# Performance work log

Measured on AMD Instinct MI355X. Metric: run time of the kernel, lower is better.

Reference implementation:

```python
import jax, jax.numpy as jnp
import numpy as np

B, N, E, H, P = 4, 512, 512, 32, 128
D = E // H
SCALING = D ** -0.5
EPS = 1e-5


def layer_norm(x, g, b):
    mu = jnp.mean(x, axis=-1, keepdims=True)
    var = jnp.var(x, axis=-1, keepdims=True)
    return (x - mu) * jax.lax.rsqrt(var + EPS) * g + b


def setup_inputs() -> dict:
    key = jax.random.key(0)
    ks = jax.random.split(key, 12)
    inp = {
        "query": jax.random.normal(ks[0], (B, N, E), jnp.float32),
        "pair": jax.random.normal(ks[1], (B, N, N, P), jnp.float32),
        "attn_mask": jnp.zeros((B, H, N, N), jnp.float32),
        "delta_pos": jax.random.normal(ks[2], (B, N, N, 3), jnp.float32),
        # parameters
        "ln_g": jnp.ones((E,), jnp.float32),
        "ln_b": jnp.zeros((E,), jnp.float32),
        "Wq": jax.random.normal(ks[3], (E, E), jnp.float32) * (1.0 / np.sqrt(E)),
        "Wk": jax.random.normal(ks[4], (E, E), jnp.float32) * (1.0 / np.sqrt(E)),
        "Wv": jax.random.normal(ks[5], (E, E), jnp.float32) * (1.0 / np.sqrt(E)),
        "pln_g": jnp.ones((P,), jnp.float32),
        "pln_b": jnp.zeros((P,), jnp.float32),
        "Wb": jax.random.normal(ks[6], (H, P), jnp.float32) * (1.0 / np.sqrt(P)),
        "bb": jnp.zeros((H,), jnp.float32),
        "Wf": jax.random.normal(ks[7], (1, E), jnp.float32) * (1.0 / np.sqrt(E)),
    }
    return inp


def reference(query, pair, attn_mask, delta_pos,
              ln_g, ln_b, Wq, Wk, Wv, pln_g, pln_b, Wb, bb, Wf):
    x = layer_norm(query, ln_g, ln_b)                       # (B,N,E)
    q = (x @ Wq.T).reshape(B, N, H, D).transpose(0, 2, 1, 3) * SCALING  # (B,H,N,D)
    k = (x @ Wk.T).reshape(B, N, H, D).transpose(0, 2, 1, 3)
    v = (x @ Wv.T).reshape(B, N, H, D).transpose(0, 2, 1, 3)
    attn = jnp.einsum('bhid,bhjd->bhij', q, k)              # (B,H,N,N)
    pair_n = layer_norm(pair, pln_g, pln_b)
    bias = (pair_n @ Wb.T + bb).transpose(0, 3, 1, 2)       # (B,H,N,N)
    attn = jax.nn.softmax(attn + bias + attn_mask, axis=-1)  # dropout off (eval)
    # rot_attn_probs: attn (B,H,N,N) * delta_pos (B,N,N,3) -> contract over j with v
    # out per (b, i, coord c, head h, d): sum_j attn[b,h,i,j]*delta_pos[b,i,j,c]*v[b,h,j,d]
    xo = jnp.einsum('bhij,bijc,bhjd->bichd', attn, delta_pos, v)  # (B,N,3,H,D)
    xo = xo.reshape(B, N, 3, E)
    cur_force = (xo @ Wf.T).reshape(B, N, 3)
    return cur_force
```

## Files before the change

kernel.cpp:

```cpp
#include <hip/hip_runtime.h>
#include <hip/hip_bf16.h>
#include <stdint.h>

constexpr int cB = 4, cN = 512, cE = 512, cH = 32, cP = 128;

typedef __attribute__((ext_vector_type(8))) short bf16x8;
typedef __attribute__((ext_vector_type(4))) float f32x4;

__device__ __forceinline__ unsigned short f2bf(float f) {
    union { float f; unsigned u; } v; v.f = f;
    unsigned u = v.u;
    u += 0x7fffu + ((u >> 16) & 1u);
    return (unsigned short)(u >> 16);
}
__device__ __forceinline__ float bf2f(unsigned short s) {
    union { unsigned u; float f; } v; v.u = ((unsigned)s) << 16;
    return v.f;
}

__global__ __launch_bounds__(256) void ln_query_kernel(
    const float* __restrict__ q, const float* __restrict__ g,
    const float* __restrict__ b, float* __restrict__ xn)
{
    int row = blockIdx.x;
    int t = threadIdx.x;
    const float* xr = q + (size_t)row * cE;
    float2 v = *(const float2*)(xr + t * 2);
    float s = v.x + v.y;
    float ss = v.x * v.x + v.y * v.y;
    #pragma unroll
    for (int o = 32; o > 0; o >>= 1) {
        s  += __shfl_down(s, o, 64);
        ss += __shfl_down(ss, o, 64);
    }
    __shared__ float red[8];
    int wv = t >> 6, ln = t & 63;
    if (ln == 0) { red[wv] = s; red[wv + 4] = ss; }
    __syncthreads();
    if (t == 0) {
        float S = red[0] + red[1] + red[2] + red[3];
        float SS = red[4] + red[5] + red[6] + red[7];
        float mu = S * (1.0f / cE);
        float var = SS * (1.0f / cE) - mu * mu;
        red[0] = mu; red[1] = rsqrtf(var + 1e-5f);
    }
    __syncthreads();
    float mu = red[0], rs = red[1];
    float2 gg = *(const float2*)(g + t * 2);
    float2 bb2 = *(const float2*)(b + t * 2);
    float2 o2;
    o2.x = (v.x - mu) * rs * gg.x + bb2.x;
    o2.y = (v.y - mu) * rs * gg.y + bb2.y;
    *(float2*)(xn + (size_t)row * cE + t * 2) = o2;
}

__global__ void setup_kernel(
    const float* __restrict__ Wb, const float* __restrict__ pg,
    const float* __restrict__ pb, const float* __restrict__ bbv,
    unsigned short* __restrict__ Wbp, float* __restrict__ Sh,
    float* __restrict__ cbh)
{
    int h = threadIdx.x;
    if (h < cH) {
        float s = 0.f, c = bbv[h];
        for (int p = 0; p < cP; ++p) {
            float wv = Wb[h * cP + p];
            float wp = wv * pg[p];
            s += wp;
            c += pb[p] * wv;
            Wbp[h * cP + p] = f2bf(wp);
        }
        Sh[h] = s; cbh[h] = c;
    }
}

__global__ __launch_bounds__(256) void qkv_kernel(
    const float* __restrict__ xn,
    const float* __restrict__ Wq, const float* __restrict__ Wk,
    const float* __restrict__ Wv, const float* __restrict__ Wf,
    float* __restrict__ Q, float* __restrict__ K, float* __restrict__ w)
{
    int mtile = blockIdx.x & 31;
    int ntile = blockIdx.x >> 5;
    int mat = ntile >> 3;
    int ncol0 = (ntile & 7) * 64;
    const float* W = (mat == 0) ? Wq : ((mat == 1) ? Wk : Wv);
    int rm = mtile * 64;
    int t = threadIdx.x;
    int tm = t >> 4, tn = t & 15;

    __shared__ float As[32][68];
    __shared__ float Bs[32][68];
    float acc[4][4];
    #pragma unroll
    for (int i = 0; i < 4; ++i)
        #pragma unroll
        for (int j = 0; j < 4; ++j) acc[i][j] = 0.f;

    for (int k0 = 0; k0 < cE; k0 += 32) {
        #pragma unroll
        for (int s = 0; s < 2; ++s) {
            int f = t + 256 * s;
            int row = f >> 3, kq = f & 7;
            float4 v = *(const float4*)(xn + (size_t)(rm + row) * cE + k0 + kq * 4);
            As[kq * 4 + 0][row] = v.x; As[kq * 4 + 1][row] = v.y;
            As[kq * 4 + 2][row] = v.z; As[kq * 4 + 3][row] = v.w;
            float4 u = *(const float4*)(W + (size_t)(ncol0 + row) * cE + k0 + kq * 4);
            Bs[kq * 4 + 0][row] = u.x; Bs[kq * 4 + 1][row] = u.y;
            Bs[kq * 4 + 2][row] = u.z; Bs[kq * 4 + 3][row] = u.w;
        }
        __syncthreads();
        #pragma unroll
        for (int kk = 0; kk < 32; ++kk) {
            float a[4], bv[4];
            #pragma unroll
            for (int i = 0; i < 4; ++i) a[i] = As[kk][tm * 4 + i];
            #pragma unroll
            for (int j = 0; j < 4; ++j) bv[j] = Bs[kk][tn * 4 + j];
            #pragma unroll
            for (int i = 0; i < 4; ++i)
                #pragma unroll
                for (int j = 0; j < 4; ++j) acc[i][j] = fmaf(a[i], bv[j], acc[i][j]);
        }
        __syncthreads();
    }

    if (mat < 2) {
        float scale = (mat == 0) ? 0.25f : 1.0f;
        float* dst = (mat == 0) ? Q : K;
        #pragma unroll
        for (int i = 0; i < 4; ++i) {
            int r = rm + tm * 4 + i;
            float4 o;
            o.x = acc[i][0] * scale; o.y = acc[i][1] * scale;
            o.z = acc[i][2] * scale; o.w = acc[i][3] * scale;
            *(float4*)(dst + (size_t)r * cE + ncol0 + tn * 4) = o;
        }
    } else {
        int col0 = ncol0 + tn * 4;
        int h = col0 >> 4;
        float wf[4];
        #pragma unroll
        for (int j = 0; j < 4; ++j) wf[j] = Wf[col0 + j];
        #pragma unroll
        for (int i = 0; i < 4; ++i) {
            int r = rm + tm * 4 + i;
            float part = 0.f;
            #pragma unroll
            for (int j = 0; j < 4; ++j) part = fmaf(acc[i][j], wf[j], part);
            atomicAdd(&w[(size_t)r * cH + h], part);
        }
    }
}

__global__ __launch_bounds__(256, 4) void attn_kernel(
    const float* __restrict__ pair, const float* __restrict__ mask,
    const float* __restrict__ dpos, const float* __restrict__ Q,
    const float* __restrict__ K, const float* __restrict__ w,
    const unsigned short* __restrict__ Wbp, const float* __restrict__ Sh_g,
    const float* __restrict__ cb_g, float* __restrict__ out)
{
    int bi = blockIdx.x;
    int b = bi >> 9, i = bi & 511;
    int t = threadIdx.x;
    int lane = t & 63, wv = t >> 6;

    __shared__ __align__(16) unsigned short Ap[64 * 136];
    __shared__ __align__(16) unsigned short Bw[32 * 136];
    __shared__ float biasT[64 * 33];
    __shared__ float mrow[64], rrow[64];
    __shared__ __align__(16) float dl2[2][192];
    __shared__ float statred[64][8];

    {
        const ushort4* src = (const ushort4*)Wbp;
        #pragma unroll
        for (int s = 0; s < 4; ++s) {
            int f = t + 256 * s;
            int hh = f >> 5, p4 = f & 31;
            ushort4 v = src[f];
            *(ushort4*)&Bw[hh * 136 + p4 * 4] = v;
        }
    }

    int h = t & 31, js = t >> 5;
    int g = js, c4 = t & 31;

    float qreg[16];
    {
        const float4* qp = (const float4*)(Q + (size_t)bi * cE + h * 16);
        #pragma unroll
        for (int d4 = 0; d4 < 4; ++d4) {
            float4 qv = qp[d4];
            qreg[d4 * 4 + 0] = qv.x; qreg[d4 * 4 + 1] = qv.y;
            qreg[d4 * 4 + 2] = qv.z; qreg[d4 * 4 + 3] = qv.w;
        }
    }
    float Sh_loc = Sh_g[h], cb_loc = cb_g[h];

    float m = -1e30f, l = 0.f, a0 = 0.f, a1 = 0.f, a2 = 0.f;

    const float* pbase = pair + (size_t)bi * cN * cP;
    const float* dbase = dpos + (size_t)bi * cN * 3;
    const float* Kbase = K + (size_t)b * cN * cE;
    const float* wbase = w + (size_t)b * cN * cH;
    const float* mbase = mask + ((size_t)(b * cH + h) * cN + i) * cN;

    float4 pf[8];
    #pragma unroll
    for (int s = 0; s < 8; ++s)
        pf[s] = *(const float4*)(pbase + (size_t)(g + 8 * s) * cP + c4 * 4);
    float4 dpf = {0.f, 0.f, 0.f, 0.f};
    if (t < 48) dpf = *(const float4*)(dbase + t * 4);

    for (int it = 0; it < 8; ++it) {
        int j0 = it * 64;
        int buf = it & 1;

        #pragma unroll
        for (int s = 0; s < 8; ++s) {
            ushort4 u;
            u.x = f2bf(pf[s].x); u.y = f2bf(pf[s].y);
            u.z = f2bf(pf[s].z); u.w = f2bf(pf[s].w);
            *(ushort4*)&Ap[(g + 8 * s) * 136 + c4 * 4] = u;
        }
        if (t < 48) *(float4*)&dl2[buf][t * 4] = dpf;

        if (it < 7) {
            const float* pb2 = pbase + (size_t)(j0 + 64) * cP;
            #pragma unroll
            for (int s = 0; s < 8; ++s)
                pf[s] = *(const float4*)(pb2 + (size_t)(g + 8 * s) * cP + c4 * 4);
            if (t < 48) dpf = *(const float4*)(dbase + (size_t)(j0 + 64) * 3 + t * 4);
        }

        float mka[8];
        {
            float4 mf0 = *(const float4*)(mbase + j0 + js * 8);
            float4 mf1 = *(const float4*)(mbase + j0 + js * 8 + 4);
            mka[0] = mf0.x; mka[1] = mf0.y; mka[2] = mf0.z; mka[3] = mf0.w;
            mka[4] = mf1.x; mka[5] = mf1.y; mka[6] = mf1.z; mka[7] = mf1.w;
        }

        __syncthreads();

        {
            int r = t >> 2, q = t & 3;
            float s1 = 0.f, s2 = 0.f;
            #pragma unroll
            for (int p = 0; p < 32; ++p) {
                float f = bf2f(Ap[r * 136 + q * 32 + p]);
                s1 += f; s2 = fmaf(f, f, s2);
            }
            statred[r][q] = s1; statred[r][q + 4] = s2;
        }

        {
            f32x4 acc0 = {0.f, 0.f, 0.f, 0.f}, acc1 = {0.f, 0.f, 0.f, 0.f};
            int arow = wv * 16 + (lane & 15);
            int kq = (lane >> 4) * 8;
            #pragma unroll
            for (int kb = 0; kb < 4; ++kb) {
                int k = kb * 32 + kq;
                bf16x8 af = *(const bf16x8*)&Ap[arow * 136 + k];
                bf16x8 b0 = *(const bf16x8*)&Bw[(lane & 15) * 136 + k];
                bf16x8 b1 = *(const bf16x8*)&Bw[(16 + (lane & 15)) * 136 + k];
                acc0 = __builtin_amdgcn_mfma_f32_16x16x32_bf16(af, b0, acc0, 0, 0, 0);
                acc1 = __builtin_amdgcn_mfma_f32_16x16x32_bf16(af, b1, acc1, 0, 0, 0);
            }
            int crow = wv * 16 + (lane >> 4) * 4;
            int ccol = lane & 15;
            #pragma unroll
            for (int r = 0; r < 4; ++r) {
                biasT[(crow + r) * 33 + ccol] = acc0[r];
                biasT[(crow + r) * 33 + 16 + ccol] = acc1[r];
            }
        }
        __syncthreads();

        if (t < 64) {
            float s1 = statred[t][0] + statred[t][1] + statred[t][2] + statred[t][3];
            float s2 = statred[t][4] + statred[t][5] + statred[t][6] + statred[t][7];
            float mu = s1 * (1.0f / cP);
            float var = s2 * (1.0f / cP) - mu * mu;
            mrow[t] = mu;
            rrow[t] = rsqrtf(var + 1e-5f);
        }
        __syncthreads();

        #pragma unroll
        for (int jj = 0; jj < 8; ++jj) {
            int jr = js * 8 + jj;
            int j = j0 + jr;
            float bias = rrow[jr] * (biasT[jr * 33 + h] - mrow[jr] * Sh_loc) + cb_loc;
            const float4* kp4 = (const float4*)(Kbase + (size_t)j * cE + h * 16);
            float qk = 0.f;
            #pragma unroll
            for (int d4 = 0; d4 < 4; ++d4) {
                float4 kv = kp4[d4];
                qk = fmaf(qreg[d4 * 4 + 0], kv.x, qk);
                qk = fmaf(qreg[d4 * 4 + 1], kv.y, qk);
                qk = fmaf(qreg[d4 * 4 + 2], kv.z, qk);
                qk = fmaf(qreg[d4 * 4 + 3], kv.w, qk);
            }
            float z = qk + bias + mka[jj];
            float wj = wbase[(size_t)j * cH + h];
            float mn = fmaxf(m, z);
            float sc = __expf(m - mn);
            float p = __expf(z - mn);
            l = l * sc + p;
            float pw = p * wj;
            a0 = fmaf(pw, dl2[buf][jr * 3 + 0], a0 * sc);
            a1 = fmaf(pw, dl2[buf][jr * 3 + 1], a1 * sc);
            a2 = fmaf(pw, dl2[buf][jr * 3 + 2], a2 * sc);
            m = mn;
        }
    }

    __syncthreads();
    float* red = biasT;
    red[(h * 8 + js) * 6 + 0] = m;
    red[(h * 8 + js) * 6 + 1] = l;
    red[(h * 8 + js) * 6 + 2] = a0;
    red[(h * 8 + js) * 6 + 3] = a1;
    red[(h * 8 + js) * 6 + 4] = a2;
    __syncthreads();
    for (int s = 4; s >= 1; s >>= 1) {
        if (js < s) {
            float* p1 = &red[(h * 8 + js) * 6];
            float* p2 = &red[(h * 8 + js + s) * 6];
            float m1 = p1[0], m2 = p2[0];
            float mn = fmaxf(m1, m2);
            float s1 = __expf(m1 - mn), s2 = __expf(m2 - mn);
            p1[0] = mn;
            p1[1] = p1[1] * s1 + p2[1] * s2;
            p1[2] = p1[2] * s1 + p2[2] * s2;
            p1[3] = p1[3] * s1 + p2[3] * s2;
            p1[4] = p1[4] * s1 + p2[4] * s2;
        }
        __syncthreads();
    }
    if (js == 0) {
        float linv = 1.0f / red[h * 48 + 1];
        biasT[1536 + h * 3 + 0] = red[h * 48 + 2] * linv;
        biasT[1536 + h * 3 + 1] = red[h * 48 + 3] * linv;
        biasT[1536 + h * 3 + 2] = red[h * 48 + 4] * linv;
    }
    __syncthreads();
    if (t < 3) {
        float s = 0.f;
        #pragma unroll
        for (int hh = 0; hh < cH; ++hh) s += biasT[1536 + hh * 3 + t];
        out[(size_t)bi * 3 + t] = s;
    }
}

extern "C" void kernel_launch(void* const* d_in, const int* in_sizes, int n_in,
                              void* d_out, int out_size, void* d_ws, size_t ws_size,
                              hipStream_t stream)
{
    const float* query = (const float*)d_in[0];
    const float* pair  = (const float*)d_in[1];
    const float* amask = (const float*)d_in[2];
    const float* dpos  = (const float*)d_in[3];
    const float* ln_g  = (const float*)d_in[4];
    const float* ln_b  = (const float*)d_in[5];
    const float* Wq    = (const float*)d_in[6];
    const float* Wk    = (const float*)d_in[7];
    const float* Wv    = (const float*)d_in[8];
    const float* pg    = (const float*)d_in[9];
    const float* pb    = (const float*)d_in[10];
    const float* Wb    = (const float*)d_in[11];
    const float* bbv   = (const float*)d_in[12];
    const float* Wf    = (const float*)d_in[13];
    float* out = (float*)d_out;

    char* ws = (char*)d_ws;
    float* xn = (float*)ws;
    float* Q  = (float*)(ws + (size_t)4 * 1048576);
    float* K  = (float*)(ws + (size_t)8 * 1048576);
    float* w  = (float*)(ws + (size_t)12 * 1048576);
    unsigned short* Wbp = (unsigned short*)(ws + (size_t)12 * 1048576 + 262144);
    float* Sh  = (float*)(ws + (size_t)12 * 1048576 + 262144 + 8192);
    float* cbh = (float*)(ws + (size_t)12 * 1048576 + 262144 + 8192 + 128);

    ln_query_kernel<<<cB * cN, 256, 0, stream>>>(query, ln_g, ln_b, xn);
    setup_kernel<<<1, 64, 0, stream>>>(Wb, pg, pb, bbv, Wbp, Sh, cbh);
    hipMemsetAsync(w, 0, (size_t)cB * cN * cH * sizeof(float), stream);
    qkv_kernel<<<32 * 24, 256, 0, stream>>>(xn, Wq, Wk, Wv, Wf, Q, K, w);
    attn_kernel<<<cB * cN, 256, 0, stream>>>(pair, amask, dpos, Q, K, w, Wbp, Sh, cbh, out);
}
```

Measured before the change: 1.012 ms.

## Replace syncthreads with non-draining barriers and prefetch mask and weights

Adds a barrier that waits only on LDS counters, so outstanding global prefetches of pair/dpos/mask stay in flight across the barrier instead of being drained by __syncthreads. The mask row is now prefetched one iteration ahead, and the per-j w values are loaded into registers early. The layernorm statistics reduction uses wave shuffles in place of a shared-memory array, which removes one barrier per iteration. The LDS stat reads are vectorized. Register pressure rises, and correctness depends on the compiler inserting vmcnt waits before the prefetched values are used.

```diff
diff --git a/kernel.cpp b/kernel.cpp
--- a/kernel.cpp
+++ b/kernel.cpp
@@ -16,6 +16,13 @@
 __device__ __forceinline__ float bf2f(unsigned short s) {
     union { unsigned u; float f; } v; v.u = ((unsigned)s) << 16;
     return v.f;
+}
+
+__device__ __forceinline__ void barrier_nodrain() {
+    asm volatile("s_waitcnt lgkmcnt(0)" ::: "memory");
+    __builtin_amdgcn_sched_barrier(0);
+    __builtin_amdgcn_s_barrier();
+    __builtin_amdgcn_sched_barrier(0);
 }
 
 __global__ __launch_bounds__(256) void ln_query_kernel(
@@ -170,7 +177,6 @@
     __shared__ float biasT[64 * 33];
     __shared__ float mrow[64], rrow[64];
     __shared__ __align__(16) float dl2[2][192];
-    __shared__ float statred[64][8];
 
     {
         const ushort4* src = (const ushort4*)Wbp;
@@ -206,6 +212,8 @@
     const float* wbase = w + (size_t)b * cN * cH;
     const float* mbase = mask + ((size_t)(b * cH + h) * cN + i) * cN;
 
+    float4 mk0 = *(const float4*)(mbase + js * 8);
+    float4 mk1 = *(const float4*)(mbase + js * 8 + 4);
     float4 pf[8];
     #pragma unroll
     for (int s = 0; s < 8; ++s)
@@ -226,7 +234,20 @@
         }
         if (t < 48) *(float4*)&dl2[buf][t * 4] = dpf;
 
+        float mka[8];
+        mka[0] = mk0.x; mka[1] = mk0.y; mka[2] = mk0.z; mka[3] = mk0.w;
+        mka[4] = mk1.x; mka[5] = mk1.y; mka[6] = mk1.z; mka[7] = mk1.w;
+
+        float wreg[8];
+        #pragma unroll
+        for (int jj = 0; jj < 8; ++jj)
+            wreg[jj] = wbase[(size_t)(j0 + js * 8 + jj) * cH + h];
+
+        __builtin_amdgcn_sched_barrier(0);
+
         if (it < 7) {
+            mk0 = *(const float4*)(mbase + j0 + 64 + js * 8);
+            mk1 = *(const float4*)(mbase + j0 + 64 + js * 8 + 4);
             const float* pb2 = pbase + (size_t)(j0 + 64) * cP;
             #pragma unroll
             for (int s = 0; s < 8; ++s)
@@ -234,27 +255,35 @@
             if (t < 48) dpf = *(const float4*)(dbase + (size_t)(j0 + 64) * 3 + t * 4);
         }
 
-        float mka[8];
-        {
-            float4 mf0 = *(const float4*)(mbase + j0 + js * 8);
-            float4 mf1 = *(const float4*)(mbase + j0 + js * 8 + 4);
-            mka[0] = mf0.x; mka[1] = mf0.y; mka[2] = mf0.z; mka[3] = mf0.w;
-            mka[4] = mf1.x; mka[5] = mf1.y; mka[6] = mf1.z; mka[7] = mf1.w;
-        }
-
-        __syncthreads();
+        barrier_nodrain();
 
         {
             int r = t >> 2, q = t & 3;
+            const uint4* apv = (const uint4*)&Ap[r * 136 + q * 32];
             float s1 = 0.f, s2 = 0.f;
             #pragma unroll
-            for (int p = 0; p < 32; ++p) {
-                float f = bf2f(Ap[r * 136 + q * 32 + p]);
-                s1 += f; s2 = fmaf(f, f, s2);
+            for (int vv = 0; vv < 4; ++vv) {
+                uint4 x = apv[vv];
+                unsigned uu[4] = {x.x, x.y, x.z, x.w};
+                #pragma unroll
+                for (int e = 0; e < 4; ++e) {
+                    union { unsigned u; float f; } lo, hi;
+                    lo.u = uu[e] << 16;
+                    hi.u = uu[e] & 0xffff0000u;
+                    s1 += lo.f + hi.f;
+                    s2 = fmaf(lo.f, lo.f, s2);
+                    s2 = fmaf(hi.f, hi.f, s2);
+                }
             }
-            statred[r][q] = s1; statred[r][q + 4] = s2;
-        }
-
+            s1 += __shfl_xor(s1, 1, 64); s2 += __shfl_xor(s2, 1, 64);
+            s1 += __shfl_xor(s1, 2, 64); s2 += __shfl_xor(s2, 2, 64);
+            if ((t & 3) == 0) {
+                float mu = s1 * (1.0f / cP);
+                float var = s2 * (1.0f / cP) - mu * mu;
+                mrow[r] = mu;
+                rrow[r] = rsqrtf(var + 1e-5f);
+            }
+        }
         {
             f32x4 acc0 = {0.f, 0.f, 0.f, 0.f}, acc1 = {0.f, 0.f, 0.f, 0.f};
             int arow = wv * 16 + (lane & 15);
@@ -276,17 +305,8 @@
                 biasT[(crow + r) * 33 + 16 + ccol] = acc1[r];
             }
         }
-        __syncthreads();
-
-        if (t < 64) {
-            float s1 = statred[t][0] + statred[t][1] + statred[t][2] + statred[t][3];
-            float s2 = statred[t][4] + statred[t][5] + statred[t][6] + statred[t][7];
-            float mu = s1 * (1.0f / cP);
-            float var = s2 * (1.0f / cP) - mu * mu;
-            mrow[t] = mu;
-            rrow[t] = rsqrtf(var + 1e-5f);
-        }
-        __syncthreads();
+
+        barrier_nodrain();
 
         #pragma unroll
         for (int jj = 0; jj < 8; ++jj) {
@@ -304,7 +324,7 @@
                 qk = fmaf(qreg[d4 * 4 + 3], kv.w, qk);
             }
             float z = qk + bias + mka[jj];
-            float wj = wbase[(size_t)j * cH + h];
+            float wj = wreg[jj];
             float mn = fmaxf(m, z);
             float sc = __expf(m - mn);
             float p = __expf(z - mn);
```

Result: slower. 1.064 ms (+5.2%).

## Stream pair tiles via global_load_lds and normalize in-tile before MFMA bias

Applied to the files above, without the earlier changes.

The attention kernel now loads 32-row pair tiles straight into LDS with global_load_lds, in place of staging them in registers. It layer-normalizes each row in fp32 before converting to bf16, so the MFMA output is the bias directly and the separate stats/mean-correction passes and extra barriers go away. Work is remapped so each thread owns one head and 4 j values from the MFMA accumulator, with mask and w values prefetched one tile ahead. Custom barriers with explicit waitcnt replace __syncthreads. The trade is more iterations (16 vs 8) and a single-buffered LDS tile that is overwritten while computing, which relies on the barrier ordering being correct.

```diff
diff --git a/kernel.cpp b/kernel.cpp
--- a/kernel.cpp
+++ b/kernel.cpp
@@ -13,9 +13,26 @@
     u += 0x7fffu + ((u >> 16) & 1u);
     return (unsigned short)(u >> 16);
 }
-__device__ __forceinline__ float bf2f(unsigned short s) {
-    union { unsigned u; float f; } v; v.u = ((unsigned)s) << 16;
-    return v.f;
+__device__ __forceinline__ unsigned pack2bf(float lo, float hi) {
+    return (unsigned)f2bf(lo) | ((unsigned)f2bf(hi) << 16);
+}
+
+#define BAR_VM() do { \
+    asm volatile("s_waitcnt vmcnt(0) lgkmcnt(0)" ::: "memory"); \
+    __builtin_amdgcn_sched_barrier(0); \
+    __builtin_amdgcn_s_barrier(); \
+    __builtin_amdgcn_sched_barrier(0); } while (0)
+
+#define BAR_LGKM() do { \
+    asm volatile("s_waitcnt lgkmcnt(0)" ::: "memory"); \
+    __builtin_amdgcn_sched_barrier(0); \
+    __builtin_amdgcn_s_barrier(); \
+    __builtin_amdgcn_sched_barrier(0); } while (0)
+
+__device__ __forceinline__ void gl_lds16(const float* g, float* l) {
+    __builtin_amdgcn_global_load_lds(
+        (const __attribute__((address_space(1))) void*)g,
+        (__attribute__((address_space(3))) void*)l, 16, 0, 0);
 }
 
 __global__ __launch_bounds__(256) void ln_query_kernel(
@@ -54,24 +71,31 @@
     *(float2*)(xn + (size_t)row * cE + t * 2) = o2;
 }
 
-__global__ void setup_kernel(
+__global__ __launch_bounds__(256) void setup_kernel(
     const float* __restrict__ Wb, const float* __restrict__ pg,
     const float* __restrict__ pb, const float* __restrict__ bbv,
     unsigned short* __restrict__ Wbp, float* __restrict__ Sh,
     float* __restrict__ cbh)
 {
-    int h = threadIdx.x;
-    if (h < cH) {
-        float s = 0.f, c = bbv[h];
-        for (int p = 0; p < cP; ++p) {
-            float wv = Wb[h * cP + p];
-            float wp = wv * pg[p];
-            s += wp;
-            c += pb[p] * wv;
-            Wbp[h * cP + p] = f2bf(wp);
-        }
-        Sh[h] = s; cbh[h] = c;
-    }
+    int t = threadIdx.x;
+    int h = t >> 3, s8 = t & 7;
+    const float* wrow = Wb + h * cP + s8 * 16;
+    const float* pgp = pg + s8 * 16;
+    const float* pbp = pb + s8 * 16;
+    unsigned short* wdst = Wbp + h * cP + s8 * 16;
+    float s = 0.f, c = 0.f;
+    #pragma unroll
+    for (int e = 0; e < 16; ++e) {
+        float wv = wrow[e];
+        float wp = wv * pgp[e];
+        s += wp;
+        c = fmaf(pbp[e], wv, c);
+        wdst[e] = f2bf(wp);
+    }
+    s += __shfl_xor(s, 1, 64); c += __shfl_xor(c, 1, 64);
+    s += __shfl_xor(s, 2, 64); c += __shfl_xor(c, 2, 64);
+    s += __shfl_xor(s, 4, 64); c += __shfl_xor(c, 4, 64);
+    if (s8 == 0) { Sh[h] = s; cbh[h] = c + bbv[h]; }
 }
 
 __global__ __launch_bounds__(256) void qkv_kernel(
@@ -165,12 +189,10 @@
     int t = threadIdx.x;
     int lane = t & 63, wv = t >> 6;
 
-    __shared__ __align__(16) unsigned short Ap[64 * 136];
+    __shared__ __align__(16) float Lf32[4096];
+    __shared__ __align__(16) unsigned short Ap[32 * 136];
     __shared__ __align__(16) unsigned short Bw[32 * 136];
-    __shared__ float biasT[64 * 33];
-    __shared__ float mrow[64], rrow[64];
-    __shared__ __align__(16) float dl2[2][192];
-    __shared__ float statred[64][8];
+    __shared__ __align__(16) float dl[2][128];
 
     {
         const ushort4* src = (const ushort4*)Wbp;
@@ -183,12 +205,14 @@
         }
     }
 
-    int h = t & 31, js = t >> 5;
-    int g = js, c4 = t & 31;
+    int j16 = (wv & 1) * 16, h16 = (wv >> 1) * 16;
+    int q4 = lane >> 4;
+    int jb = j16 + q4 * 4;
+    int hT = h16 + (lane & 15);
 
     float qreg[16];
     {
-        const float4* qp = (const float4*)(Q + (size_t)bi * cE + h * 16);
+        const float4* qp = (const float4*)(Q + (size_t)bi * cE + hT * 16);
         #pragma unroll
         for (int d4 = 0; d4 < 4; ++d4) {
             float4 qv = qp[d4];
@@ -196,7 +220,7 @@
             qreg[d4 * 4 + 2] = qv.z; qreg[d4 * 4 + 3] = qv.w;
         }
     }
-    float Sh_loc = Sh_g[h], cb_loc = cb_g[h];
+    float cb_loc = cb_g[hT];
 
     float m = -1e30f, l = 0.f, a0 = 0.f, a1 = 0.f, a2 = 0.f;
 
@@ -204,96 +228,101 @@
     const float* dbase = dpos + (size_t)bi * cN * 3;
     const float* Kbase = K + (size_t)b * cN * cE;
     const float* wbase = w + (size_t)b * cN * cH;
-    const float* mbase = mask + ((size_t)(b * cH + h) * cN + i) * cN;
-
-    float4 pf[8];
+    const float* mbase = mask + ((size_t)(b * cH + hT) * cN + i) * cN;
+
+    float4 mka = *(const float4*)(mbase + jb);
+    float wcur[4];
     #pragma unroll
-    for (int s = 0; s < 8; ++s)
-        pf[s] = *(const float4*)(pbase + (size_t)(g + 8 * s) * cP + c4 * 4);
+    for (int jj = 0; jj < 4; ++jj)
+        wcur[jj] = wbase[(size_t)(jb + jj) * cH + hT];
     float4 dpf = {0.f, 0.f, 0.f, 0.f};
-    if (t < 48) dpf = *(const float4*)(dbase + t * 4);
-
-    for (int it = 0; it < 8; ++it) {
-        int j0 = it * 64;
-        int buf = it & 1;
-
-        #pragma unroll
-        for (int s = 0; s < 8; ++s) {
-            ushort4 u;
-            u.x = f2bf(pf[s].x); u.y = f2bf(pf[s].y);
-            u.z = f2bf(pf[s].z); u.w = f2bf(pf[s].w);
-            *(ushort4*)&Ap[(g + 8 * s) * 136 + c4 * 4] = u;
-        }
-        if (t < 48) *(float4*)&dl2[buf][t * 4] = dpf;
-
-        if (it < 7) {
-            const float* pb2 = pbase + (size_t)(j0 + 64) * cP;
-            #pragma unroll
-            for (int s = 0; s < 8; ++s)
-                pf[s] = *(const float4*)(pb2 + (size_t)(g + 8 * s) * cP + c4 * 4);
-            if (t < 48) dpf = *(const float4*)(dbase + (size_t)(j0 + 64) * 3 + t * 4);
-        }
-
-        float mka[8];
+    if (t < 24) dpf = *(const float4*)(dbase + t * 4);
+    #pragma unroll
+    for (int s = 0; s < 4; ++s) {
+        int chunk = wv * 4 + s;
+        gl_lds16(pbase + chunk * 256 + lane * 4, &Lf32[chunk * 256]);
+    }
+
+    int buf = 0;
+    for (int it = 0; it < 16; ++it) {
+        const int j0 = it * 32;
+
+        if (t < 24) *(float4*)&dl[buf][t * 4] = dpf;
+
+        BAR_VM();
+
         {
-            float4 mf0 = *(const float4*)(mbase + j0 + js * 8);
-            float4 mf1 = *(const float4*)(mbase + j0 + js * 8 + 4);
-            mka[0] = mf0.x; mka[1] = mf0.y; mka[2] = mf0.z; mka[3] = mf0.w;
-            mka[4] = mf1.x; mka[5] = mf1.y; mka[6] = mf1.z; mka[7] = mf1.w;
-        }
-
-        __syncthreads();
-
+            int r = t >> 3, sub = t & 7;
+            const float4* lr = (const float4*)&Lf32[r * 128 + sub * 16];
+            float4 x0 = lr[0], x1 = lr[1], x2 = lr[2], x3 = lr[3];
+            float s1 = x0.x + x0.y + x0.z + x0.w + x1.x + x1.y + x1.z + x1.w
+                     + x2.x + x2.y + x2.z + x2.w + x3.x + x3.y + x3.z + x3.w;
+            float s2 = 0.f;
+            s2 = fmaf(x0.x, x0.x, s2); s2 = fmaf(x0.y, x0.y, s2);
+            s2 = fmaf(x0.z, x0.z, s2); s2 = fmaf(x0.w, x0.w, s2);
+            s2 = fmaf(x1.x, x1.x, s2); s2 = fmaf(x1.y, x1.y, s2);
+            s2 = fmaf(x1.z, x1.z, s2); s2 = fmaf(x1.w, x1.w, s2);
+            s2 = fmaf(x2.x, x2.x, s2); s2 = fmaf(x2.y, x2.y, s2);
+            s2 = fmaf(x2.z, x2.z, s2); s2 = fmaf(x2.w, x2.w, s2);
+            s2 = fmaf(x3.x, x3.x, s2); s2 = fmaf(x3.y, x3.y, s2);
+            s2 = fmaf(x3.z, x3.z, s2); s2 = fmaf(x3.w, x3.w, s2);
+            s1 += __shfl_xor(s1, 1, 64); s2 += __shfl_xor(s2, 1, 64);
+            s1 += __shfl_xor(s1, 2, 64); s2 += __shfl_xor(s2, 2, 64);
+            s1 += __shfl_xor(s1, 4, 64); s2 += __shfl_xor(s2, 4, 64);
+            float mu = s1 * (1.0f / cP);
+            float rs_ = rsqrtf(s2 * (1.0f / cP) - mu * mu + 1e-5f);
+            uint4 o0, o1;
+            o0.x = pack2bf((x0.x - mu) * rs_, (x0.y - mu) * rs_);
+            o0.y = pack2bf((x0.z - mu) * rs_, (x0.w - mu) * rs_);
+            o0.z = pack2bf((x1.x - mu) * rs_, (x1.y - mu) * rs_);
+            o0.w = pack2bf((x1.z - mu) * rs_, (x1.w - mu) * rs_);
+            o1.x = pack2bf((x2.x - mu) * rs_, (x2.y - mu) * rs_);
+            o1.y = pack2bf((x2.z - mu) * rs_, (x2.w - mu) * rs_);
+            o1.z = pack2bf((x3.x - mu) * rs_, (x3.y - mu) * rs_);
+            o1.w = pack2bf((x3.z - mu) * rs_, (x3.w - mu) * rs_);
+            *(uint4*)&Ap[r * 136 + sub * 16] = o0;
+            *(uint4*)&Ap[r * 136 + sub * 16 + 8] = o1;
+        }
+
+        BAR_LGKM();
+
+        float4 mk_n = {0.f, 0.f, 0.f, 0.f};
+        float wn0 = 0.f, wn1 = 0.f, wn2 = 0.f, wn3 = 0.f;
+        if (it < 15) {
+            const float* slab = pbase + (size_t)(j0 + 32) * cP;
+            #pragma unroll
+            for (int s = 0; s < 4; ++s) {
+                int chunk = wv * 4 + s;
+                gl_lds16(slab + chunk * 256 + lane * 4, &Lf32[chunk * 256]);
+            }
+            mk_n = *(const float4*)(mbase + j0 + 32 + jb);
+            wn0 = wbase[(size_t)(j0 + 32 + jb + 0) * cH + hT];
+            wn1 = wbase[(size_t)(j0 + 32 + jb + 1) * cH + hT];
+            wn2 = wbase[(size_t)(j0 + 32 + jb + 2) * cH + hT];
+            wn3 = wbase[(size_t)(j0 + 32 + jb + 3) * cH + hT];
+            if (t < 24) dpf = *(const float4*)(dbase + (size_t)(j0 + 32) * 3 + t * 4);
+        }
+
+        f32x4 acc = {0.f, 0.f, 0.f, 0.f};
         {
-            int r = t >> 2, q = t & 3;
-            float s1 = 0.f, s2 = 0.f;
-            #pragma unroll
-            for (int p = 0; p < 32; ++p) {
-                float f = bf2f(Ap[r * 136 + q * 32 + p]);
-                s1 += f; s2 = fmaf(f, f, s2);
-            }
-            statred[r][q] = s1; statred[r][q + 4] = s2;
-        }
-
-        {
-            f32x4 acc0 = {0.f, 0.f, 0.f, 0.f}, acc1 = {0.f, 0.f, 0.f, 0.f};
-            int arow = wv * 16 + (lane & 15);
-            int kq = (lane >> 4) * 8;
+            int ar = (j16 + (lane & 15)) * 136;
+            int br = (h16 + (lane & 15)) * 136;
+            int kq = q4 * 8;
             #pragma unroll
             for (int kb = 0; kb < 4; ++kb) {
                 int k = kb * 32 + kq;
-                bf16x8 af = *(const bf16x8*)&Ap[arow * 136 + k];
-                bf16x8 b0 = *(const bf16x8*)&Bw[(lane & 15) * 136 + k];
-                bf16x8 b1 = *(const bf16x8*)&Bw[(16 + (lane & 15)) * 136 + k];
-                acc0 = __builtin_amdgcn_mfma_f32_16x16x32_bf16(af, b0, acc0, 0, 0, 0);
-                acc1 = __builtin_amdgcn_mfma_f32_16x16x32_bf16(af, b1, acc1, 0, 0, 0);
+                bf16x8 af = *(const bf16x8*)&Ap[ar + k];
+                bf16x8 bb_ = *(const bf16x8*)&Bw[br + k];
+                acc = __builtin_amdgcn_mfma_f32_16x16x32_bf16(af, bb_, acc, 0, 0, 0);
             }
-            int crow = wv * 16 + (lane >> 4) * 4;
-            int ccol = lane & 15;
-            #pragma unroll
-            for (int r = 0; r < 4; ++r) {
-                biasT[(crow + r) * 33 + ccol] = acc0[r];
-                biasT[(crow + r) * 33 + 16 + ccol] = acc1[r];
-            }
-        }
-        __syncthreads();
-
-        if (t < 64) {
-            float s1 = statred[t][0] + statred[t][1] + statred[t][2] + statred[t][3];
-            float s2 = statred[t][4] + statred[t][5] + statred[t][6] + statred[t][7];
-            float mu = s1 * (1.0f / cP);
-            float var = s2 * (1.0f / cP) - mu * mu;
-            mrow[t] = mu;
-            rrow[t] = rsqrtf(var + 1e-5f);
-        }
-        __syncthreads();
-
-        #pragma unroll
-        for (int jj = 0; jj < 8; ++jj) {
-            int jr = js * 8 + jj;
+        }
+
+        #pragma unroll
+        for (int jj = 0; jj < 4; ++jj) {
+            int jr = jb + jj;
             int j = j0 + jr;
-            float bias = rrow[jr] * (biasT[jr * 33 + h] - mrow[jr] * Sh_loc) + cb_loc;
-            const float4* kp4 = (const float4*)(Kbase + (size_t)j * cE + h * 16);
+            float bias = acc[jj] + cb_loc;
+            const float4* kp4 = (const float4*)(Kbase + (size_t)j * cE + hT * 16);
             float qk = 0.f;
             #pragma unroll
             for (int d4 = 0; d4 < 4; ++d4) {
@@ -303,32 +332,38 @@
                 qk = fmaf(qreg[d4 * 4 + 2], kv.z, qk);
                 qk = fmaf(qreg[d4 * 4 + 3], kv.w, qk);
             }
-            float z = qk + bias + mka[jj];
-            float wj = wbase[(size_t)j * cH + h];
+            float mkv = (jj == 0) ? mka.x : (jj == 1) ? mka.y : (jj == 2) ? mka.z : mka.w;
+            float z = qk + bias + mkv;
+            float wj = wcur[jj];
             float mn = fmaxf(m, z);
             float sc = __expf(m - mn);
             float p = __expf(z - mn);
             l = l * sc + p;
             float pw = p * wj;
-            a0 = fmaf(pw, dl2[buf][jr * 3 + 0], a0 * sc);
-            a1 = fmaf(pw, dl2[buf][jr * 3 + 1], a1 * sc);
-            a2 = fmaf(pw, dl2[buf][jr * 3 + 2], a2 * sc);
+            a0 = fmaf(pw, dl[buf][jr * 3 + 0], a0 * sc);
+            a1 = fmaf(pw, dl[buf][jr * 3 + 1], a1 * sc);
+            a2 = fmaf(pw, dl[buf][jr * 3 + 2], a2 * sc);
             m = mn;
         }
-    }
-
-    __syncthreads();
-    float* red = biasT;
-    red[(h * 8 + js) * 6 + 0] = m;
-    red[(h * 8 + js) * 6 + 1] = l;
-    red[(h * 8 + js) * 6 + 2] = a0;
-    red[(h * 8 + js) * 6 + 3] = a1;
-    red[(h * 8 + js) * 6 + 4] = a2;
+        if (it < 15) {
+            mka = mk_n;
+            wcur[0] = wn0; wcur[1] = wn1; wcur[2] = wn2; wcur[3] = wn3;
+        }
+        buf ^= 1;
+    }
+
+    float* red = Lf32;
+    int slice = (wv & 1) * 4 + q4;
+    red[(hT * 8 + slice) * 6 + 0] = m;
+    red[(hT * 8 + slice) * 6 + 1] = l;
+    red[(hT * 8 + slice) * 6 + 2] = a0;
+    red[(hT * 8 + slice) * 6 + 3] = a1;
+    red[(hT * 8 + slice) * 6 + 4] = a2;
     __syncthreads();
     for (int s = 4; s >= 1; s >>= 1) {
-        if (js < s) {
-            float* p1 = &red[(h * 8 + js) * 6];
-            float* p2 = &red[(h * 8 + js + s) * 6];
+        if (slice < s) {
+            float* p1 = &red[(hT * 8 + slice) * 6];
+            float* p2 = &red[(hT * 8 + slice + s) * 6];
             float m1 = p1[0], m2 = p2[0];
             float mn = fmaxf(m1, m2);
             float s1 = __expf(m1 - mn), s2 = __expf(m2 - mn);
@@ -340,17 +375,17 @@
         }
         __syncthreads();
     }
-    if (js == 0) {
-        float linv = 1.0f / red[h * 48 + 1];
-        biasT[1536 + h * 3 + 0] = red[h * 48 + 2] * linv;
-        biasT[1536 + h * 3 + 1] = red[h * 48 + 3] * linv;
-        biasT[1536 + h * 3 + 2] = red[h * 48 + 4] * linv;
+    if (slice == 0) {
+        float linv = 1.0f / red[hT * 48 + 1];
+        red[2048 + hT * 3 + 0] = red[hT * 48 + 2] * linv;
+        red[2048 + hT * 3 + 1] = red[hT * 48 + 3] * linv;
+        red[2048 + hT * 3 + 2] = red[hT * 48 + 4] * linv;
     }
     __syncthreads();
     if (t < 3) {
         float s = 0.f;
         #pragma unroll
-        for (int hh = 0; hh < cH; ++hh) s += biasT[1536 + hh * 3 + t];
+        for (int hh = 0; hh < cH; ++hh) s += red[2048 + hh * 3 + t];
         out[(size_t)bi * 3 + t] = s;
     }
 }
@@ -385,7 +420,7 @@
     float* cbh = (float*)(ws + (size_t)12 * 1048576 + 262144 + 8192 + 128);
 
     ln_query_kernel<<<cB * cN, 256, 0, stream>>>(query, ln_g, ln_b, xn);
-    setup_kernel<<<1, 64, 0, stream>>>(Wb, pg, pb, bbv, Wbp, Sh, cbh);
+    setup_kernel<<<1, 256, 0, stream>>>(Wb, pg, pb, bbv, Wbp, Sh, cbh);
     hipMemsetAsync(w, 0, (size_t)cB * cN * cH * sizeof(float), stream);
     qkv_kernel<<<32 * 24, 256, 0, stream>>>(xn, Wq, Wk, Wv, Wf, Q, K, w);
     attn_kernel<<<cB * cN, 256, 0, stream>>>(pair, amask, dpos, Q, K, w, Wbp, Sh, cbh, out);
```

After: 923.5 us. -8.7%, faster.
